# Kernel tuning notes

Measured on AMD Instinct MI355X. Metric: run time of the kernel, lower is better.

## Reference

```python
import jax, jax.numpy as jnp
import numpy as np

D_MODEL = 256   # dim // 2
DIM = 512
D_INNER = 512   # expand=2 * d_model
D_STATE = 16
D_CONV = 4
DT_RANK = 16    # ceil(d_model/16)
N_LAYERS = 2
H_RES, W_RES = 16, 16
EPS = 1e-5


def silu(v):
    return v * jax.nn.sigmoid(v)


def setup_inputs() -> dict:
    key = jax.random.key(0)
    ks = jax.random.split(key, 12)
    Bsz, T, N = 2, 4, 256
    x = jax.random.normal(ks[0], (Bsz, 1 + T * N, DIM), jnp.float32)
    skip = jax.random.normal(ks[1], (Bsz, 1 + 4 * T * N, D_MODEL), jnp.float32)
    sc = lambda k, shape, s: jax.random.normal(k, shape, jnp.float32) * s
    exp_w = sc(ks[2], (2 * DIM, DIM), 0.02)            # PatchExpanding2D.expansion (no bias)
    ln_g = jnp.ones((DIM // 2,), jnp.float32)
    ln_b = jnp.zeros((DIM // 2,), jnp.float32)
    cls_w = sc(ks[3], (DIM // 2, DIM), 0.02)
    cls_b = jnp.zeros((DIM // 2,), jnp.float32)
    in_proj_w = sc(ks[4], (N_LAYERS, 2 * D_INNER, D_MODEL), 0.02)
    conv_w = sc(ks[5], (N_LAYERS, D_INNER, D_CONV), 0.1)  # depthwise causal conv
    conv_b = jnp.zeros((N_LAYERS, D_INNER), jnp.float32)
    xproj_w = sc(ks[6], (N_LAYERS, DT_RANK + 2 * D_STATE, D_INNER), 0.02)
    dt_w = sc(ks[7], (N_LAYERS, D_INNER, DT_RANK), 0.1)
    dt_b = sc(ks[8], (N_LAYERS, D_INNER), 0.1)
    A_log = jnp.log(jnp.broadcast_to(jnp.arange(1, D_STATE + 1, dtype=jnp.float32), (N_LAYERS, D_INNER, D_STATE)))
    Dp = jnp.ones((N_LAYERS, D_INNER), jnp.float32)
    out_w = sc(ks[9], (N_LAYERS, D_MODEL, D_INNER), 0.02)
    bn_g = jnp.ones((D_MODEL,), jnp.float32)
    bn_b = jnp.zeros((D_MODEL,), jnp.float32)
    return {"x": x, "skip_connection": skip, "exp_w": exp_w, "ln_g": ln_g, "ln_b": ln_b,
            "cls_w": cls_w, "cls_b": cls_b, "in_proj_w": in_proj_w, "conv_w": conv_w,
            "conv_b": conv_b, "xproj_w": xproj_w, "dt_w": dt_w, "dt_b": dt_b,
            "A_log": A_log, "Dp": Dp, "out_w": out_w, "bn_g": bn_g, "bn_b": bn_b,
            "B": 2, "T": 4, "N": 256}


def mamba_layer(u, Wi, cw, cb, Wx, Wdt, bdt, A_log, Dd, Wo):
    # u: [B, L, d_model]
    Bb, L, _ = u.shape
    xz = jnp.einsum('bld,ed->ble', u, Wi)            # [B, L, 2*d_inner]
    xi, z = jnp.split(xz, 2, axis=-1)
    # depthwise causal conv1d (pad left d_conv-1)
    xp = jnp.pad(xi, ((0, 0), (D_CONV - 1, 0), (0, 0)))
    xc = cb + sum(cw[:, k] * xp[:, k:k + L, :] for k in range(D_CONV))
    xi = silu(xc)
    dbc = jnp.einsum('bld,ed->ble', xi, Wx)          # [B, L, dt_rank + 2*d_state]
    dt = dbc[..., :DT_RANK]
    Bm = dbc[..., DT_RANK:DT_RANK + D_STATE]
    Cm = dbc[..., DT_RANK + D_STATE:]
    delta = jax.nn.softplus(jnp.einsum('blr,dr->bld', dt, Wdt) + bdt)  # [B, L, d_inner]
    A = -jnp.exp(A_log)                              # [d_inner, d_state]

    def step(h, inp):
        d_t, B_t, C_t, x_t = inp                     # [B,d], [B,n], [B,n], [B,d]
        h = h * jnp.exp(d_t[..., None] * A) + d_t[..., None] * B_t[:, None, :] * x_t[..., None]
        y = jnp.einsum('bdn,bn->bd', h, C_t)
        return h, y

    h0 = jnp.zeros((Bb, D_INNER, D_STATE), u.dtype)
    xs = (jnp.swapaxes(delta, 0, 1), jnp.swapaxes(Bm, 0, 1),
          jnp.swapaxes(Cm, 0, 1), jnp.swapaxes(xi, 0, 1))
    _, ys = jax.lax.scan(step, h0, xs)               # ys: [L, B, d_inner]
    y = jnp.swapaxes(ys, 0, 1) + xi * Dd
    y = y * silu(z)
    return jnp.einsum('bld,od->blo', y, Wo)          # [B, L, d_model]


def reference(x, skip_connection, exp_w, ln_g, ln_b, cls_w, cls_b, in_proj_w, conv_w,
              conv_b, xproj_w, dt_w, dt_b, A_log, Dp, out_w, bn_g, bn_b, B, T, N):
    cls = x[:B, :1, :]                               # [B, 1, dim]
    toks = x[:, 1:, :].reshape(x.shape[0], T, N, DIM)
    # patch expanding: Linear dim -> 2*dim, then 2x2 pixel shuffle, LayerNorm(dim//2)
    e = jnp.einsum('btnm,em->btne', toks, exp_w)     # [B, T, N, 2*dim]
    m = (2 * DIM) // 4                               # dim // 2
    e = e.reshape(-1, T, H_RES, W_RES, 2, 2, m)
    e = jnp.transpose(e, (0, 1, 2, 4, 3, 5, 6)).reshape(-1, T, 4 * N, m)
    mu = e.mean(-1, keepdims=True)
    var = e.var(-1, keepdims=True)
    e = (e - mu) / jnp.sqrt(var + EPS) * ln_g + ln_b
    e = e.reshape(e.shape[0], T * 4 * N, m)
    cls = jnp.einsum('bom,em->boe', cls, cls_w) + cls_b
    xx = jnp.concatenate([cls, e], axis=1) + skip_connection
    for i in range(N_LAYERS):
        xx = mamba_layer(xx, in_proj_w[i], conv_w[i], conv_b[i], xproj_w[i],
                         dt_w[i], dt_b[i], A_log[i], Dp[i], out_w[i])
    # BatchNorm1d over channels (training-mode batch stats, biased variance)
    mu = xx.mean(axis=(0, 1))
    var = xx.var(axis=(0, 1))
    xx = (xx - mu) / jnp.sqrt(var + EPS) * bn_g + bn_b
    return xx, 4 * N
```

## Files before the change

kernel.cpp:

```cpp
#include <hip/hip_runtime.h>
#include <hip/hip_bf16.h>
#include <math.h>

#define L_TOT 4097
#define BSZ 2
#define ROWS (BSZ*L_TOT)
#define NSEG 64
#define SEGLEN 65

typedef __bf16 bf16x8 __attribute__((ext_vector_type(8)));
typedef float  f32x4  __attribute__((ext_vector_type(4)));
#define ASTR 56
#define AST2 72

__device__ __forceinline__ float sigmoidf_(float v){ return 1.0f/(1.0f+__expf(-v)); }
__device__ __forceinline__ float siluf_(float v){ return v * sigmoidf_(v); }
__device__ __forceinline__ unsigned short bfbits(float f){
    __bf16 h = (__bf16)f;
    return __builtin_bit_cast(unsigned short, h);
}

__global__ __launch_bounds__(256) void prep_all(
    const float* __restrict__ w0, const float* __restrict__ w1,
    const float* __restrict__ w2, const float* __restrict__ w3,
    const float* __restrict__ x,
    __bf16* __restrict__ o0, __bf16* __restrict__ o1,
    __bf16* __restrict__ o2, __bf16* __restrict__ o3,
    __bf16* __restrict__ gx, float* __restrict__ stats)
{
    const int bid = blockIdx.x;
    if (bid < 664) {
        long i = ((long)bid*256 + threadIdx.x)*8;
        const float* src; __bf16* dst; long off;
        if (i < 524288)        { src = w0; dst = o0; off = i; }
        else if (i < 1048576)  { src = w1; dst = o1; off = i - 524288; }
        else if (i < 1310720)  { src = w2; dst = o2; off = i - 1048576; }
        else                   { src = w3; dst = o3; off = i - 1310720; }
        float4 a = *(const float4*)(src+off), b = *(const float4*)(src+off+4);
        bf16x8 o;
        o[0]=(__bf16)a.x; o[1]=(__bf16)a.y; o[2]=(__bf16)a.z; o[3]=(__bf16)a.w;
        o[4]=(__bf16)b.x; o[5]=(__bf16)b.y; o[6]=(__bf16)b.z; o[7]=(__bf16)b.w;
        *(bf16x8*)(dst+off) = o;
        return;
    }
    if (bid == 664) {
        stats[threadIdx.x] = 0.f;
        stats[threadIdx.x + 256] = 0.f;
    }
    long i = ((long)(bid-664)*256 + threadIdx.x)*8;
    if (i >= 2048L*512) return;
    int row = (int)(i >> 9), col = (int)(i & 511);
    long srow = row + (row >> 10) + 1;
    const float* src = x + srow*512 + col;
    float4 a = *(const float4*)src, b = *(const float4*)(src+4);
    bf16x8 o;
    o[0]=(__bf16)a.x; o[1]=(__bf16)a.y; o[2]=(__bf16)a.z; o[3]=(__bf16)a.w;
    o[4]=(__bf16)b.x; o[5]=(__bf16)b.y; o[6]=(__bf16)b.z; o[7]=(__bf16)b.w;
    *(bf16x8*)(gx+i) = o;
}

__global__ __launch_bounds__(256) void gemm_bf16(
    const __bf16* __restrict__ A, const __bf16* __restrict__ W,
    __bf16* __restrict__ C2, int M, int N, int K)
{
    __shared__ __bf16 Als[128*ASTR];
    __shared__ __bf16 Wls[64*ASTR];
    const int tid = threadIdx.x;
    const int lane = tid & 63, w = tid >> 6;
    const int n0 = blockIdx.x*64, m0 = blockIdx.y*128;

    f32x4 acc[2][4] = {};
    const int arow = tid >> 1, ahalf = tid & 1;
    const int wrow = tid >> 2, wseg = tid & 3;
    const int fr = lane & 15, fc = lane >> 4;

    for (int k0 = 0; k0 < K; k0 += 32) {
        bf16x8 av0 = {}, av1 = {};
        if (m0 + arow < M) {
            const __bf16* src = A + (long)(m0+arow)*K + k0 + ahalf*16;
            av0 = *(const bf16x8*)src;
            av1 = *(const bf16x8*)(src+8);
        }
        bf16x8 wv = *(const bf16x8*)(W + (long)(n0+wrow)*K + k0 + wseg*8);
        __syncthreads();
        *(bf16x8*)&Als[arow*ASTR + ahalf*16]     = av0;
        *(bf16x8*)&Als[arow*ASTR + ahalf*16 + 8] = av1;
        *(bf16x8*)&Wls[wrow*ASTR + wseg*8]       = wv;
        __syncthreads();

        bf16x8 a0 = *(const bf16x8*)&Als[(w*32 +      fr)*ASTR + fc*8];
        bf16x8 a1 = *(const bf16x8*)&Als[(w*32 + 16 + fr)*ASTR + fc*8];
        #pragma unroll
        for (int j = 0; j < 4; j++) {
            bf16x8 bv = *(const bf16x8*)&Wls[(j*16 + fr)*ASTR + fc*8];
            acc[0][j] = __builtin_amdgcn_mfma_f32_16x16x32_bf16(a0, bv, acc[0][j], 0,0,0);
            acc[1][j] = __builtin_amdgcn_mfma_f32_16x16x32_bf16(a1, bv, acc[1][j], 0,0,0);
        }
    }
    #pragma unroll
    for (int i = 0; i < 2; i++) {
        #pragma unroll
        for (int rr = 0; rr < 4; rr++) {
            int grow = m0 + w*32 + i*16 + fc*4 + rr;
            if (grow < M) {
                #pragma unroll
                for (int j = 0; j < 4; j++)
                    C2[(long)grow*N + n0 + j*16 + fr] = (__bf16)acc[i][j][rr];
            }
        }
    }
}

__global__ __launch_bounds__(256) void gemm_inproj(
    const __bf16* __restrict__ A, const __bf16* __restrict__ W,
    __bf16* __restrict__ xhb, __bf16* __restrict__ zsb, int M, int K)
{
    __shared__ __bf16 Als[128*AST2];
    __shared__ __bf16 Wls[128*AST2];
    const int tid = threadIdx.x;
    const int lane = tid & 63, w = tid >> 6;
    const int n0 = blockIdx.x*128, m0 = blockIdx.y*128;
    const int fr = lane & 15, fc = lane >> 4;
    const int row2 = tid >> 1, half = tid & 1;

    f32x4 acc[2][8] = {};

    for (int k0 = 0; k0 < K; k0 += 64) {
        bf16x8 av[4], wv[4];
        const bool aok = (m0 + row2) < M;
        const __bf16* asrc = A + (long)(m0+row2)*K + k0 + half*32;
        const __bf16* wsrc = W + (long)(n0+row2)*K + k0 + half*32;
        #pragma unroll
        for (int e = 0; e < 4; e++) {
            av[e] = aok ? *(const bf16x8*)(asrc + e*8) : (bf16x8){};
            wv[e] = *(const bf16x8*)(wsrc + e*8);
        }
        __syncthreads();
        #pragma unroll
        for (int e = 0; e < 4; e++) {
            *(bf16x8*)&Als[row2*AST2 + half*32 + e*8] = av[e];
            *(bf16x8*)&Wls[row2*AST2 + half*32 + e*8] = wv[e];
        }
        __syncthreads();
        #pragma unroll
        for (int s = 0; s < 2; s++) {
            bf16x8 a0 = *(const bf16x8*)&Als[(w*32 +      fr)*AST2 + s*32 + fc*8];
            bf16x8 a1 = *(const bf16x8*)&Als[(w*32 + 16 + fr)*AST2 + s*32 + fc*8];
            #pragma unroll
            for (int j = 0; j < 8; j++) {
                bf16x8 bv = *(const bf16x8*)&Wls[(j*16 + fr)*AST2 + s*32 + fc*8];
                acc[0][j] = __builtin_amdgcn_mfma_f32_16x16x32_bf16(a0, bv, acc[0][j], 0,0,0);
                acc[1][j] = __builtin_amdgcn_mfma_f32_16x16x32_bf16(a1, bv, acc[1][j], 0,0,0);
            }
        }
    }
    const bool xhalf = (n0 < 512);
    const int cbase = xhalf ? n0 : (n0 - 512);
    #pragma unroll
    for (int i = 0; i < 2; i++) {
        #pragma unroll
        for (int rr = 0; rr < 4; rr++) {
            int grow = m0 + w*32 + i*16 + fc*4 + rr;
            if (grow < M) {
                if (xhalf) {
                    #pragma unroll
                    for (int j = 0; j < 8; j++)
                        xhb[(long)grow*512 + cbase + j*16 + fr] = (__bf16)acc[i][j][rr];
                } else {
                    #pragma unroll
                    for (int j = 0; j < 8; j++)
                        zsb[(long)grow*512 + cbase + j*16 + fr] = (__bf16)siluf_(acc[i][j][rr]);
                }
            }
        }
    }
}

__global__ __launch_bounds__(256) void gemm_dbc(
    const __bf16* __restrict__ A, const __bf16* __restrict__ W,
    float* __restrict__ dt16, float* __restrict__ BC, int M)
{
    __shared__ __bf16 Als[64*ASTR];
    __shared__ __bf16 Wls[48*ASTR];
    const int tid = threadIdx.x;
    const int lane = tid & 63, w = tid >> 6;
    const int m0 = blockIdx.x*64;
    f32x4 acc[3] = {};

    const int arow = tid >> 2, aseg = tid & 3;
    const int fr = lane & 15, fc = lane >> 4;

    for (int k0 = 0; k0 < 512; k0 += 32) {
        bf16x8 av = {};
        if (m0 + arow < M)
            av = *(const bf16x8*)(A + (long)(m0+arow)*512 + k0 + aseg*8);
        bf16x8 wv = {};
        if (tid < 192)
            wv = *(const bf16x8*)(W + (long)(tid>>2)*512 + k0 + (tid&3)*8);
        __syncthreads();
        *(bf16x8*)&Als[arow*ASTR + aseg*8] = av;
        if (tid < 192) *(bf16x8*)&Wls[(tid>>2)*ASTR + (tid&3)*8] = wv;
        __syncthreads();

        bf16x8 a0 = *(const bf16x8*)&Als[(w*16 + fr)*ASTR + fc*8];
        #pragma unroll
        for (int j = 0; j < 3; j++) {
            bf16x8 bv = *(const bf16x8*)&Wls[(j*16 + fr)*ASTR + fc*8];
            acc[j] = __builtin_amdgcn_mfma_f32_16x16x32_bf16(a0, bv, acc[j], 0,0,0);
        }
    }
    #pragma unroll
    for (int rr = 0; rr < 4; rr++) {
        long grow = m0 + w*16 + fc*4 + rr;
        if (grow < M) {
            dt16[grow*16 + fr]    = acc[0][rr];
            BC[grow*32 + fr]      = acc[1][rr];
            BC[grow*32 + 16 + fr] = acc[2][rr];
        }
    }
}

__global__ __launch_bounds__(256) void delta_k(
    const float* __restrict__ dt16, const float* __restrict__ Wdt,
    const float* __restrict__ bdt, const __bf16* __restrict__ xib,
    unsigned* __restrict__ pdx)
{
    __shared__ float dtS[8*16];
    const int tid = threadIdx.x;
    const long r0 = (long)blockIdx.x*8;
    if (tid < 32) {
        long idx = r0*16 + tid*4;
        f32x4 v = (idx < (long)ROWS*16) ? *(const f32x4*)&dt16[idx] : (f32x4){};
        *(f32x4*)&dtS[tid*4] = v;
    }
    const int d0 = tid, d1 = tid + 256;
    f32x4 wa[4], wb[4];
    #pragma unroll
    for (int q = 0; q < 4; q++) {
        wa[q] = *(const f32x4*)(Wdt + d0*16 + q*4);
        wb[q] = *(const f32x4*)(Wdt + d1*16 + q*4);
    }
    const float b0 = bdt[d0], b1 = bdt[d1];
    __syncthreads();
    #pragma unroll
    for (int rr = 0; rr < 8; rr++) {
        long row = r0 + rr;
        if (row >= ROWS) return;
        const float* dt = &dtS[rr*16];
        float s0 = b0, s1 = b1;
        #pragma unroll
        for (int e = 0; e < 4; e++) {
            s0 += wa[0][e]*dt[e] + wa[1][e]*dt[4+e] + wa[2][e]*dt[8+e] + wa[3][e]*dt[12+e];
            s1 += wb[0][e]*dt[e] + wb[1][e]*dt[4+e] + wb[2][e]*dt[8+e] + wb[3][e]*dt[12+e];
        }
        float dl0 = (s0 > 20.f) ? s0 : log1pf(__expf(s0));
        float dl1 = (s1 > 20.f) ? s1 : log1pf(__expf(s1));
        unsigned x0 = __builtin_bit_cast(unsigned short, xib[row*512 + d0]);
        unsigned x1 = __builtin_bit_cast(unsigned short, xib[row*512 + d1]);
        pdx[row*512 + d0] = (unsigned)bfbits(dl0) | (x0 << 16);
        pdx[row*512 + d1] = (unsigned)bfbits(dl1) | (x1 << 16);
    }
}

__global__ __launch_bounds__(256) void rearrange_ln_cls(
    const __bf16* __restrict__ e_buf, const float* __restrict__ x,
    const float* __restrict__ cls_w, const float* __restrict__ cls_b,
    const float* __restrict__ ln_g, const float* __restrict__ ln_b,
    const float* __restrict__ skip, __bf16* __restrict__ xxb)
{
    const int wv = threadIdx.x >> 6, lane = threadIdx.x & 63;
    if (blockIdx.x >= 2048) {
        const int widx = (blockIdx.x - 2048)*4 + wv;
        const int b = widx >> 8, c = widx & 255;
        const float* xr = x + (long)b*1025*512 + lane*8;
        const float* wr = cls_w + (long)c*512 + lane*8;
        float4 xa = *(const float4*)xr,  xb4 = *(const float4*)(xr+4);
        float4 wa = *(const float4*)wr,  wb4 = *(const float4*)(wr+4);
        float s = xa.x*wa.x + xa.y*wa.y + xa.z*wa.z + xa.w*wa.w
                + xb4.x*wb4.x + xb4.y*wb4.y + xb4.z*wb4.z + xb4.w*wb4.w;
        #pragma unroll
        for (int o = 32; o > 0; o >>= 1) s += __shfl_xor(s, o);
        if (lane == 0) {
            long o = (long)b*L_TOT*256 + c;
            xxb[o] = (__bf16)(s + cls_b[c] + skip[o]);
        }
        return;
    }
    const int qg = blockIdx.x*4 + wv;
    const int b = qg >> 12, q = (qg & 4095) + 1;
    const long obase = ((long)b*L_TOT + q)*256;

    const int t  = (q-1) >> 10;
    const int p  = (q-1) & 1023;
    const int h  = p >> 6;
    const int a  = (p >> 5) & 1;
    const int w_ = (p >> 1) & 15;
    const int bb = p & 1;
    const long tok = (long)b*1024 + t*256 + h*16 + w_;
    const __bf16* src = e_buf + tok*1024 + a*512 + bb*256 + lane*4;
    float v[4];
    {
        ushort2 u0 = *(const ushort2*)src;
        ushort2 u1 = *(const ushort2*)(src+2);
        v[0] = (float)__builtin_bit_cast(__bf16, u0.x);
        v[1] = (float)__builtin_bit_cast(__bf16, u0.y);
        v[2] = (float)__builtin_bit_cast(__bf16, u1.x);
        v[3] = (float)__builtin_bit_cast(__bf16, u1.y);
    }
    float s = v[0]+v[1]+v[2]+v[3];
    float s2 = v[0]*v[0]+v[1]*v[1]+v[2]*v[2]+v[3]*v[3];
    #pragma unroll
    for (int o = 32; o > 0; o >>= 1) { s += __shfl_xor(s, o); s2 += __shfl_xor(s2, o); }
    float mu = s * (1.f/256.f);
    float rs = rsqrtf(s2*(1.f/256.f) - mu*mu + 1e-5f);
    const int c0 = lane*4;
    float4 sk = *(const float4*)&skip[obase + c0];
    float skv[4] = {sk.x, sk.y, sk.z, sk.w};
    __bf16 ov[4];
    #pragma unroll
    for (int i = 0; i < 4; i++)
        ov[i] = (__bf16)((v[i] - mu)*rs*ln_g[c0+i] + ln_b[c0+i] + skv[i]);
    *(ushort2*)&xxb[obase + c0]     = make_ushort2(
        __builtin_bit_cast(unsigned short, ov[0]),
        __builtin_bit_cast(unsigned short, ov[1]));
    *(ushort2*)&xxb[obase + c0 + 2] = make_ushort2(
        __builtin_bit_cast(unsigned short, ov[2]),
        __builtin_bit_cast(unsigned short, ov[3]));
}

__global__ __launch_bounds__(256) void conv_silu(
    const __bf16* __restrict__ xhb, const float* __restrict__ cw,
    const float* __restrict__ cb, __bf16* __restrict__ xib)
{
    const int tid = threadIdx.x;
    const int c = tid & 63;
    const long r0 = ((long)blockIdx.x*4 + (tid >> 6))*8;
    if (r0 >= ROWS) return;
    const int d0 = c*8;
    float wreg[4][8], breg[8];
    #pragma unroll
    for (int e = 0; e < 8; e++) {
        breg[e] = cb[d0+e];
        #pragma unroll
        for (int k = 0; k < 4; k++) wreg[k][e] = cw[(d0+e)*4 + k];
    }
    bf16x8 win[4];
    #pragma unroll
    for (int j = 0; j < 3; j++) {
        long rr = r0 - 3 + j;
        win[j] = (rr >= 0) ? *(const bf16x8*)&xhb[rr*512 + d0] : (bf16x8){};
    }
    #pragma unroll
    for (int rr = 0; rr < 8; rr++) {
        long rl = r0 + rr;
        if (rl >= ROWS) break;
        win[3] = *(const bf16x8*)&xhb[rl*512 + d0];
        int l = (int)(rl % L_TOT);
        float acc[8];
        #pragma unroll
        for (int e = 0; e < 8; e++) acc[e] = breg[e];
        #pragma unroll
        for (int k = 0; k < 4; k++) {
            if (l + k - 3 >= 0) {
                #pragma unroll
                for (int e = 0; e < 8; e++)
                    acc[e] += wreg[k][e]*(float)win[k][e];
            }
        }
        bf16x8 o;
        #pragma unroll
        for (int e = 0; e < 8; e++) o[e] = (__bf16)siluf_(acc[e]);
        *(bf16x8*)&xib[rl*512 + d0] = o;
        win[0] = win[1]; win[1] = win[2]; win[2] = win[3];
    }
}

__global__ __launch_bounds__(256) void scan_p1(
    const unsigned* __restrict__ pdx,
    const float* __restrict__ BC, const float* __restrict__ A_log,
    float* __restrict__ segH, float* __restrict__ segP)
{
    __shared__ unsigned pdxS[SEGLEN*64];
    __shared__ float bS[SEGLEN*16];
    const int blk = blockIdx.x;
    const int seg = blk >> 4;
    const int b   = (blk >> 3) & 1;
    const int dbase = (blk & 7)*64;
    const int tid = threadIdx.x;
    const int l0 = seg*SEGLEN;
    const int nl = min(l0 + SEGLEN, L_TOT) - l0;
    const int nlc = nl > 0 ? nl : 0;

    for (int cc = tid; cc < nlc*16; cc += 256) {
        int l = cc >> 4, qq = cc & 15;
        *(uint4*)&pdxS[l*64 + qq*4] =
            *(const uint4*)&pdx[((long)b*L_TOT + l0 + l)*512 + dbase + qq*4];
    }
    for (int cc = tid; cc < nlc*4; cc += 256) {
        int l = cc >> 2, qq = cc & 3;
        *(f32x4*)&bS[l*16 + qq*4] =
            *(const f32x4*)&BC[((long)b*L_TOT + l0 + l)*32 + qq*4];
    }
    __syncthreads();

    const int dl_ = tid >> 2;
    const int d = dbase + dl_;
    const int ng = tid & 3;
    f32x4 Al = *(const f32x4*)(A_log + d*16 + ng*4);
    float Ar[4] = {-__expf(Al[0]), -__expf(Al[1]), -__expf(Al[2]), -__expf(Al[3])};
    float h[4] = {0,0,0,0};
    float P[4] = {1,1,1,1};
    for (int l = 0; l < nlc; l++) {
        unsigned v = pdxS[l*64 + dl_];
        float dl = __uint_as_float(v << 16);
        float xv = __uint_as_float(v & 0xffff0000u);
        f32x4 Bv = *(const f32x4*)&bS[l*16 + ng*4];
        float dx = dl*xv;
        #pragma unroll
        for (int n = 0; n < 4; n++) {
            float E = __expf(dl*Ar[n]);
            h[n] = h[n]*E + dx*Bv[n];
            P[n] *= E;
        }
    }
    long off = ((long)(seg*2 + b)*512 + d)*16 + ng*4;
    *(f32x4*)&segH[off] = f32x4{h[0],h[1],h[2],h[3]};
    *(f32x4*)&segP[off] = f32x4{P[0],P[1],P[2],P[3]};
}

__global__ __launch_bounds__(256) void scan_p2(
    float* __restrict__ segH, const float* __restrict__ segP)
{
    const int idx = blockIdx.x*256 + threadIdx.x;
    float carry = 0.f;
    for (int s0 = 0; s0 < NSEG; s0 += 8) {
        float hh[8], pp[8];
        #pragma unroll
        for (int j = 0; j < 8; j++) {
            long o = (long)(s0+j)*16384 + idx;
            hh[j] = segH[o]; pp[j] = segP[o];
        }
        #pragma unroll
        for (int j = 0; j < 8; j++) {
            long o = (long)(s0+j)*16384 + idx;
            segH[o] = carry;
            carry = pp[j]*carry + hh[j];
        }
    }
}

__global__ __launch_bounds__(256) void scan_p3(
    const unsigned* __restrict__ pdx,
    const float* __restrict__ BC, const float* __restrict__ A_log,
    const float* __restrict__ segH, const float* __restrict__ Dp,
    const __bf16* __restrict__ zsb, __bf16* __restrict__ yb)
{
    __shared__ unsigned pdxS[SEGLEN*64];
    __shared__ float bcS[SEGLEN*32];
    __shared__ __bf16 zS[SEGLEN*64];
    const int blk = blockIdx.x;
    const int seg = blk >> 4;
    const int b   = (blk >> 3) & 1;
    const int dbase = (blk & 7)*64;
    const int tid = threadIdx.x;
    const int l0 = seg*SEGLEN;
    const int nl = min(l0 + SEGLEN, L_TOT) - l0;
    const int nlc = nl > 0 ? nl : 0;
    if (nlc == 0) return;

    for (int cc = tid; cc < nlc*16; cc += 256) {
        int l = cc >> 4, qq = cc & 15;
        *(uint4*)&pdxS[l*64 + qq*4] =
            *(const uint4*)&pdx[((long)b*L_TOT + l0 + l)*512 + dbase + qq*4];
    }
    for (int cc = tid; cc < nlc*8; cc += 256) {
        int l = cc >> 3, qq = cc & 7;
        *(f32x4*)&bcS[l*32 + qq*4] =
            *(const f32x4*)&BC[((long)b*L_TOT + l0 + l)*32 + qq*4];
    }
    for (int cc = tid; cc < nlc*8; cc += 256) {
        int l = cc >> 3, qq = cc & 7;
        *(bf16x8*)&zS[l*64 + qq*8] =
            *(const bf16x8*)&zsb[((long)b*L_TOT + l0 + l)*512 + dbase + qq*8];
    }
    __syncthreads();

    const int dl_ = tid >> 2;
    const int d = dbase + dl_;
    const int ng = tid & 3;
    f32x4 Al = *(const f32x4*)(A_log + d*16 + ng*4);
    float Ar[4] = {-__expf(Al[0]), -__expf(Al[1]), -__expf(Al[2]), -__expf(Al[3])};
    long off = ((long)(seg*2 + b)*512 + d)*16 + ng*4;
    f32x4 h4 = *(const f32x4*)&segH[off];
    float h[4] = {h4[0], h4[1], h4[2], h4[3]};
    const float Dd = Dp[d];
    for (int l = 0; l < nlc; l++) {
        unsigned v = pdxS[l*64 + dl_];
        float dl = __uint_as_float(v << 16);
        float xv = __uint_as_float(v & 0xffff0000u);
        f32x4 Bv = *(const f32x4*)&bcS[l*32 + ng*4];
        f32x4 Cv = *(const f32x4*)&bcS[l*32 + 16 + ng*4];
        float dx = dl*xv;
        float y = 0.f;
        #pragma unroll
        for (int n = 0; n < 4; n++) {
            float E = __expf(dl*Ar[n]);
            h[n] = h[n]*E + dx*Bv[n];
            y += h[n]*Cv[n];
        }
        y += __shfl_xor(y, 1);
        y += __shfl_xor(y, 2);
        if (ng == 0) {
            float z = (float)zS[l*64 + dl_];
            ((unsigned short*)&pdxS[l*64 + dl_])[0] = bfbits((y + xv*Dd)*z);
        }
    }
    __syncthreads();
    for (int cc = tid; cc < nlc*8; cc += 256) {
        int l = cc >> 3, qq = cc & 7;
        bf16x8 o;
        #pragma unroll
        for (int e = 0; e < 8; e++)
            o[e] = __builtin_bit_cast(__bf16,
                       (unsigned short)(pdxS[l*64 + qq*8 + e] & 0xffffu));
        *(bf16x8*)&yb[((long)b*L_TOT + l0 + l)*512 + dbase + qq*8] = o;
    }
}

__global__ __launch_bounds__(256) void bn_reduce(
    const __bf16* __restrict__ xxb, float* __restrict__ stats)
{
    const int c = threadIdx.x;
    float s = 0.f, s2 = 0.f;
    for (int r = blockIdx.x; r < ROWS; r += gridDim.x) {
        float v = (float)xxb[(long)r*256 + c];
        s += v; s2 += v*v;
    }
    atomicAdd(&stats[c], s);
    atomicAdd(&stats[256 + c], s2);
}

__global__ __launch_bounds__(256) void bn_apply(
    const __bf16* __restrict__ xxb, const float* __restrict__ stats,
    const float* __restrict__ g, const float* __restrict__ bta,
    float* __restrict__ out)
{
    long idx = (long)blockIdx.x*256 + threadIdx.x;
    if (idx == 0) out[(long)ROWS*256] = 1024.0f;
    if (idx >= (long)ROWS*256) return;
    int c = (int)(idx & 255);
    float mu = stats[c] * (1.f/ROWS);
    float var = stats[256 + c] * (1.f/ROWS) - mu*mu;
    out[idx] = ((float)xxb[idx] - mu)*rsqrtf(var + 1e-5f)*g[c] + bta[c];
}

extern "C" void kernel_launch(void* const* d_in, const int* in_sizes, int n_in,
                              void* d_out, int out_size, void* d_ws, size_t ws_size,
                              hipStream_t stream)
{
    const float* x        = (const float*)d_in[0];
    const float* skip     = (const float*)d_in[1];
    const float* exp_w    = (const float*)d_in[2];
    const float* ln_g     = (const float*)d_in[3];
    const float* ln_b     = (const float*)d_in[4];
    const float* cls_w    = (const float*)d_in[5];
    const float* cls_b    = (const float*)d_in[6];
    const float* in_proj_w= (const float*)d_in[7];
    const float* conv_w   = (const float*)d_in[8];
    const float* conv_b   = (const float*)d_in[9];
    const float* xproj_w  = (const float*)d_in[10];
    const float* dt_w     = (const float*)d_in[11];
    const float* dt_b     = (const float*)d_in[12];
    const float* A_log    = (const float*)d_in[13];
    const float* Dp       = (const float*)d_in[14];
    const float* out_w    = (const float*)d_in[15];
    const float* bn_g     = (const float*)d_in[16];
    const float* bn_b     = (const float*)d_in[17];

    float* ws = (float*)d_ws;
    float* BC    = ws;
    float* dt16  = BC + 262208;
    float* segH  = dt16 + 131104;
    float* segP  = segH + 1048576;
    float* stats = segP + 1048576;
    unsigned* pdx = (unsigned*)(stats + 512);
    __bf16* expWb = (__bf16*)(pdx + 4195328);
    __bf16* inWb  = expWb + 524288;
    __bf16* outWb = inWb + 524288;
    __bf16* xpWb  = outWb + 262144;
    __bf16* xxb   = xpWb + 49152;
    __bf16* xhb   = xxb + 2097664;
    __bf16* e_b   = xhb;
    __bf16* zsb   = xhb + 4195328;
    __bf16* xib   = zsb + 4195328;
    __bf16* Axb   = xib;
    __bf16* yb    = xib + 4195328;
    float* out    = (float*)d_out;

    prep_all<<<1176, 256, 0, stream>>>(
        exp_w, in_proj_w, out_w, xproj_w, x,
        expWb, inWb, outWb, xpWb, Axb, stats);

    gemm_bf16<<<dim3(16, 16), 256, 0, stream>>>(
        Axb, expWb, e_b, 2048, 1024, 512);
    rearrange_ln_cls<<<2176, 256, 0, stream>>>(
        e_b, x, cls_w, cls_b, ln_g, ln_b, skip, xxb);

    for (int layer = 0; layer < 2; layer++) {
        gemm_inproj<<<dim3(8, 65), 256, 0, stream>>>(
            xxb, inWb + layer*262144, xhb, zsb, ROWS, 256);
        conv_silu<<<(ROWS + 31)/32, 256, 0, stream>>>(
            xhb, conv_w + layer*512*4, conv_b + layer*512, xib);
        gemm_dbc<<<(ROWS + 63)/64, 256, 0, stream>>>(
            xib, xpWb + layer*24576, dt16, BC, ROWS);
        delta_k<<<(ROWS + 7)/8, 256, 0, stream>>>(
            dt16, dt_w + layer*512*16, dt_b + layer*512, xib, pdx);
        scan_p1<<<NSEG*16, 256, 0, stream>>>(
            pdx, BC, A_log + layer*512*16, segH, segP);
        scan_p2<<<64, 256, 0, stream>>>(segH, segP);
        scan_p3<<<NSEG*16, 256, 0, stream>>>(
            pdx, BC, A_log + layer*512*16, segH, Dp + layer*512, zsb, yb);
        gemm_bf16<<<dim3(4, 65), 256, 0, stream>>>(
            yb, outWb + layer*131072, xxb, ROWS, 256, 512);
    }

    bn_reduce<<<128, 256, 0, stream>>>(xxb, stats);
    bn_apply<<<((long)ROWS*256 + 255)/256 + 1, 256, 0, stream>>>(
        xxb, stats, bn_g, bn_b, out);
}
```

Measured before the change: 376.7 us.

## Fuse delta softplus into scan kernels and move cls projection into prep

```diff
diff --git a/kernel.cpp b/kernel.cpp
--- a/kernel.cpp
+++ b/kernel.cpp
@@ -24,9 +24,12 @@
     const float* __restrict__ w0, const float* __restrict__ w1,
     const float* __restrict__ w2, const float* __restrict__ w3,
     const float* __restrict__ x,
+    const float* __restrict__ cls_w, const float* __restrict__ cls_b,
+    const float* __restrict__ skip,
     __bf16* __restrict__ o0, __bf16* __restrict__ o1,
     __bf16* __restrict__ o2, __bf16* __restrict__ o3,
-    __bf16* __restrict__ gx, float* __restrict__ stats)
+    __bf16* __restrict__ gx, float* __restrict__ stats,
+    __bf16* __restrict__ xxb)
 {
     const int bid = blockIdx.x;
     if (bid < 664) {
@@ -43,6 +46,24 @@
         *(bf16x8*)(dst+off) = o;
         return;
     }
+    if (bid >= 1176) {
+        const int wv = threadIdx.x >> 6, lane = threadIdx.x & 63;
+        const int widx = (bid - 1176)*4 + wv;
+        const int b = widx >> 8, c = widx & 255;
+        const float* xr = x + (long)b*1025*512 + lane*8;
+        const float* wr = cls_w + (long)c*512 + lane*8;
+        float4 xa = *(const float4*)xr,  xb4 = *(const float4*)(xr+4);
+        float4 wa = *(const float4*)wr,  wb4 = *(const float4*)(wr+4);
+        float s = xa.x*wa.x + xa.y*wa.y + xa.z*wa.z + xa.w*wa.w
+                + xb4.x*wb4.x + xb4.y*wb4.y + xb4.z*wb4.z + xb4.w*wb4.w;
+        #pragma unroll
+        for (int o = 32; o > 0; o >>= 1) s += __shfl_xor(s, o);
+        if (lane == 0) {
+            long o = (long)b*L_TOT*256 + c;
+            xxb[o] = (__bf16)(s + cls_b[c] + skip[o]);
+        }
+        return;
+    }
     if (bid == 664) {
         stats[threadIdx.x] = 0.f;
         stats[threadIdx.x + 256] = 0.f;
@@ -220,72 +241,12 @@
     }
 }
 
-__global__ __launch_bounds__(256) void delta_k(
-    const float* __restrict__ dt16, const float* __restrict__ Wdt,
-    const float* __restrict__ bdt, const __bf16* __restrict__ xib,
-    unsigned* __restrict__ pdx)
-{
-    __shared__ float dtS[8*16];
-    const int tid = threadIdx.x;
-    const long r0 = (long)blockIdx.x*8;
-    if (tid < 32) {
-        long idx = r0*16 + tid*4;
-        f32x4 v = (idx < (long)ROWS*16) ? *(const f32x4*)&dt16[idx] : (f32x4){};
-        *(f32x4*)&dtS[tid*4] = v;
-    }
-    const int d0 = tid, d1 = tid + 256;
-    f32x4 wa[4], wb[4];
-    #pragma unroll
-    for (int q = 0; q < 4; q++) {
-        wa[q] = *(const f32x4*)(Wdt + d0*16 + q*4);
-        wb[q] = *(const f32x4*)(Wdt + d1*16 + q*4);
-    }
-    const float b0 = bdt[d0], b1 = bdt[d1];
-    __syncthreads();
-    #pragma unroll
-    for (int rr = 0; rr < 8; rr++) {
-        long row = r0 + rr;
-        if (row >= ROWS) return;
-        const float* dt = &dtS[rr*16];
-        float s0 = b0, s1 = b1;
-        #pragma unroll
-        for (int e = 0; e < 4; e++) {
-            s0 += wa[0][e]*dt[e] + wa[1][e]*dt[4+e] + wa[2][e]*dt[8+e] + wa[3][e]*dt[12+e];
-            s1 += wb[0][e]*dt[e] + wb[1][e]*dt[4+e] + wb[2][e]*dt[8+e] + wb[3][e]*dt[12+e];
-        }
-        float dl0 = (s0 > 20.f) ? s0 : log1pf(__expf(s0));
-        float dl1 = (s1 > 20.f) ? s1 : log1pf(__expf(s1));
-        unsigned x0 = __builtin_bit_cast(unsigned short, xib[row*512 + d0]);
-        unsigned x1 = __builtin_bit_cast(unsigned short, xib[row*512 + d1]);
-        pdx[row*512 + d0] = (unsigned)bfbits(dl0) | (x0 << 16);
-        pdx[row*512 + d1] = (unsigned)bfbits(dl1) | (x1 << 16);
-    }
-}
-
-__global__ __launch_bounds__(256) void rearrange_ln_cls(
-    const __bf16* __restrict__ e_buf, const float* __restrict__ x,
-    const float* __restrict__ cls_w, const float* __restrict__ cls_b,
-    const float* __restrict__ ln_g, const float* __restrict__ ln_b,
-    const float* __restrict__ skip, __bf16* __restrict__ xxb)
+__global__ __launch_bounds__(256) void rearrange_ln(
+    const __bf16* __restrict__ e_buf, const float* __restrict__ ln_g,
+    const float* __restrict__ ln_b, const float* __restrict__ skip,
+    __bf16* __restrict__ xxb)
 {
     const int wv = threadIdx.x >> 6, lane = threadIdx.x & 63;
-    if (blockIdx.x >= 2048) {
-        const int widx = (blockIdx.x - 2048)*4 + wv;
-        const int b = widx >> 8, c = widx & 255;
-        const float* xr = x + (long)b*1025*512 + lane*8;
-        const float* wr = cls_w + (long)c*512 + lane*8;
-        float4 xa = *(const float4*)xr,  xb4 = *(const float4*)(xr+4);
-        float4 wa = *(const float4*)wr,  wb4 = *(const float4*)(wr+4);
-        float s = xa.x*wa.x + xa.y*wa.y + xa.z*wa.z + xa.w*wa.w
-                + xb4.x*wb4.x + xb4.y*wb4.y + xb4.z*wb4.z + xb4.w*wb4.w;
-        #pragma unroll
-        for (int o = 32; o > 0; o >>= 1) s += __shfl_xor(s, o);
-        if (lane == 0) {
-            long o = (long)b*L_TOT*256 + c;
-            xxb[o] = (__bf16)(s + cls_b[c] + skip[o]);
-        }
-        return;
-    }
     const int qg = blockIdx.x*4 + wv;
     const int b = qg >> 12, q = (qg & 4095) + 1;
     const long obase = ((long)b*L_TOT + q)*256;
@@ -376,11 +337,13 @@
 }
 
 __global__ __launch_bounds__(256) void scan_p1(
-    const unsigned* __restrict__ pdx,
+    const __bf16* __restrict__ xib, const float* __restrict__ dt16,
+    const float* __restrict__ Wdt, const float* __restrict__ bdt,
     const float* __restrict__ BC, const float* __restrict__ A_log,
     float* __restrict__ segH, float* __restrict__ segP)
 {
     __shared__ unsigned pdxS[SEGLEN*64];
+    __shared__ float dtS[SEGLEN*16];
     __shared__ float bS[SEGLEN*16];
     const int blk = blockIdx.x;
     const int seg = blk >> 4;
@@ -391,15 +354,38 @@
     const int nl = min(l0 + SEGLEN, L_TOT) - l0;
     const int nlc = nl > 0 ? nl : 0;
 
-    for (int cc = tid; cc < nlc*16; cc += 256) {
-        int l = cc >> 4, qq = cc & 15;
-        *(uint4*)&pdxS[l*64 + qq*4] =
-            *(const uint4*)&pdx[((long)b*L_TOT + l0 + l)*512 + dbase + qq*4];
+    for (int cc = tid; cc < nlc*8; cc += 256) {
+        int l = cc >> 3, qq = cc & 7;
+        bf16x8 v = *(const bf16x8*)&xib[((long)b*L_TOT + l0 + l)*512 + dbase + qq*8];
+        #pragma unroll
+        for (int e = 0; e < 8; e++)
+            pdxS[l*64 + qq*8 + e] =
+                ((unsigned)__builtin_bit_cast(unsigned short, v[e])) << 16;
+    }
+    for (int cc = tid; cc < nlc*4; cc += 256) {
+        int l = cc >> 2, qq = cc & 3;
+        *(f32x4*)&dtS[l*16 + qq*4] =
+            *(const f32x4*)&dt16[((long)b*L_TOT + l0 + l)*16 + qq*4];
     }
     for (int cc = tid; cc < nlc*4; cc += 256) {
         int l = cc >> 2, qq = cc & 3;
         *(f32x4*)&bS[l*16 + qq*4] =
             *(const f32x4*)&BC[((long)b*L_TOT + l0 + l)*32 + qq*4];
+    }
+    __syncthreads();
+    for (int cc = tid; cc < nlc*64; cc += 256) {
+        int l = cc >> 6, dl_ = cc & 63;
+        int d = dbase + dl_;
+        const f32x4* wd = (const f32x4*)(Wdt + d*16);
+        f32x4 w0 = wd[0], w1 = wd[1], w2 = wd[2], w3 = wd[3];
+        const f32x4* dt = (const f32x4*)&dtS[l*16];
+        f32x4 t0 = dt[0], t1 = dt[1], t2 = dt[2], t3 = dt[3];
+        float s = bdt[d];
+        #pragma unroll
+        for (int e = 0; e < 4; e++)
+            s += w0[e]*t0[e] + w1[e]*t1[e] + w2[e]*t2[e] + w3[e]*t3[e];
+        float dl = (s > 20.f) ? s : log1pf(__expf(s));
+        pdxS[l*64 + dl_] |= (unsigned)bfbits(dl);
     }
     __syncthreads();
 
@@ -450,12 +436,14 @@
 }
 
 __global__ __launch_bounds__(256) void scan_p3(
-    const unsigned* __restrict__ pdx,
+    const __bf16* __restrict__ xib, const float* __restrict__ dt16,
+    const float* __restrict__ Wdt, const float* __restrict__ bdt,
     const float* __restrict__ BC, const float* __restrict__ A_log,
     const float* __restrict__ segH, const float* __restrict__ Dp,
     const __bf16* __restrict__ zsb, __bf16* __restrict__ yb)
 {
     __shared__ unsigned pdxS[SEGLEN*64];
+    __shared__ float dtS[SEGLEN*16];
     __shared__ float bcS[SEGLEN*32];
     __shared__ __bf16 zS[SEGLEN*64];
     const int blk = blockIdx.x;
@@ -468,10 +456,18 @@
     const int nlc = nl > 0 ? nl : 0;
     if (nlc == 0) return;
 
-    for (int cc = tid; cc < nlc*16; cc += 256) {
-        int l = cc >> 4, qq = cc & 15;
-        *(uint4*)&pdxS[l*64 + qq*4] =
-            *(const uint4*)&pdx[((long)b*L_TOT + l0 + l)*512 + dbase + qq*4];
+    for (int cc = tid; cc < nlc*8; cc += 256) {
+        int l = cc >> 3, qq = cc & 7;
+        bf16x8 v = *(const bf16x8*)&xib[((long)b*L_TOT + l0 + l)*512 + dbase + qq*8];
+        #pragma unroll
+        for (int e = 0; e < 8; e++)
+            pdxS[l*64 + qq*8 + e] =
+                ((unsigned)__builtin_bit_cast(unsigned short, v[e])) << 16;
+    }
+    for (int cc = tid; cc < nlc*4; cc += 256) {
+        int l = cc >> 2, qq = cc & 3;
+        *(f32x4*)&dtS[l*16 + qq*4] =
+            *(const f32x4*)&dt16[((long)b*L_TOT + l0 + l)*16 + qq*4];
     }
     for (int cc = tid; cc < nlc*8; cc += 256) {
         int l = cc >> 3, qq = cc & 7;
@@ -482,6 +478,21 @@
         int l = cc >> 3, qq = cc & 7;
         *(bf16x8*)&zS[l*64 + qq*8] =
             *(const bf16x8*)&zsb[((long)b*L_TOT + l0 + l)*512 + dbase + qq*8];
+    }
+    __syncthreads();
+    for (int cc = tid; cc < nlc*64; cc += 256) {
+        int l = cc >> 6, dl_ = cc & 63;
+        int d = dbase + dl_;
+        const f32x4* wd = (const f32x4*)(Wdt + d*16);
+        f32x4 w0 = wd[0], w1 = wd[1], w2 = wd[2], w3 = wd[3];
+        const f32x4* dt = (const f32x4*)&dtS[l*16];
+        f32x4 t0 = dt[0], t1 = dt[1], t2 = dt[2], t3 = dt[3];
+        float s = bdt[d];
+        #pragma unroll
+        for (int e = 0; e < 4; e++)
+            s += w0[e]*t0[e] + w1[e]*t1[e] + w2[e]*t2[e] + w3[e]*t3[e];
+        float dl = (s > 20.f) ? s : log1pf(__expf(s));
+        pdxS[l*64 + dl_] |= (unsigned)bfbits(dl);
     }
     __syncthreads();
 
@@ -583,8 +594,7 @@
     float* segH  = dt16 + 131104;
     float* segP  = segH + 1048576;
     float* stats = segP + 1048576;
-    unsigned* pdx = (unsigned*)(stats + 512);
-    __bf16* expWb = (__bf16*)(pdx + 4195328);
+    __bf16* expWb = (__bf16*)(stats + 512);
     __bf16* inWb  = expWb + 524288;
     __bf16* outWb = inWb + 524288;
     __bf16* xpWb  = outWb + 262144;
@@ -597,14 +607,13 @@
     __bf16* yb    = xib + 4195328;
     float* out    = (float*)d_out;
 
-    prep_all<<<1176, 256, 0, stream>>>(
-        exp_w, in_proj_w, out_w, xproj_w, x,
-        expWb, inWb, outWb, xpWb, Axb, stats);
+    prep_all<<<1304, 256, 0, stream>>>(
+        exp_w, in_proj_w, out_w, xproj_w, x, cls_w, cls_b, skip,
+        expWb, inWb, outWb, xpWb, Axb, stats, xxb);
 
     gemm_bf16<<<dim3(16, 16), 256, 0, stream>>>(
         Axb, expWb, e_b, 2048, 1024, 512);
-    rearrange_ln_cls<<<2176, 256, 0, stream>>>(
-        e_b, x, cls_w, cls_b, ln_g, ln_b, skip, xxb);
+    rearrange_ln<<<2048, 256, 0, stream>>>(e_b, ln_g, ln_b, skip, xxb);
 
     for (int layer = 0; layer < 2; layer++) {
         gemm_inproj<<<dim3(8, 65), 256, 0, stream>>>(
@@ -613,18 +622,18 @@
             xhb, conv_w + layer*512*4, conv_b + layer*512, xib);
         gemm_dbc<<<(ROWS + 63)/64, 256, 0, stream>>>(
             xib, xpWb + layer*24576, dt16, BC, ROWS);
-        delta_k<<<(ROWS + 7)/8, 256, 0, stream>>>(
-            dt16, dt_w + layer*512*16, dt_b + layer*512, xib, pdx);
         scan_p1<<<NSEG*16, 256, 0, stream>>>(
-            pdx, BC, A_log + layer*512*16, segH, segP);
+            xib, dt16, dt_w + layer*512*16, dt_b + layer*512,
+            BC, A_log + layer*512*16, segH, segP);
         scan_p2<<<64, 256, 0, stream>>>(segH, segP);
         scan_p3<<<NSEG*16, 256, 0, stream>>>(
-            pdx, BC, A_log + layer*512*16, segH, Dp + layer*512, zsb, yb);
+            xib, dt16, dt_w + layer*512*16, dt_b + layer*512,
+            BC, A_log + layer*512*16, segH, Dp + layer*512, zsb, yb);
         gemm_bf16<<<dim3(4, 65), 256, 0, stream>>>(
             yb, outWb + layer*131072, xxb, ROWS, 256, 512);
     }
 
-    bn_reduce<<<128, 256, 0, stream>>>(xxb, stats);
+    bn_reduce<<<256, 256, 0, stream>>>(xxb, stats);
     bn_apply<<<((long)ROWS*256 + 255)/256 + 1, 256, 0, stream>>>(
         xxb, stats, bn_g, bn_b, out);
 }
```

Measured after the change: 391.0 us. 3.8% more time.
